# Optimization experiments

Hardware: AMD Instinct MI355X
Metric: run time of the kernel (lower is better)

Reference implementation:

```python
import jax, jax.numpy as jnp
import numpy as np

N = 100000
E = 1600000
F_IN = 3
H = 64


def setup_inputs() -> dict:
    key = jax.random.key(0)
    ks = jax.random.split(key, 12)
    x = jax.random.normal(ks[0], (N, F_IN), dtype=jnp.float32)
    edge_index = jax.random.randint(ks[1], (2, E), 0, N, dtype=jnp.int64)
    def glorot(k, fi, fo):
        s = jnp.sqrt(6.0 / (fi + fo)).astype(jnp.float32)
        return jax.random.uniform(k, (fi, fo), jnp.float32, -s, s)
    return {
        "x": x,
        "edge_index": edge_index,
        "W1": glorot(ks[2], F_IN, H), "b1": jnp.zeros((H,), jnp.float32),
        "W2": glorot(ks[3], H, H),   "b2": jnp.zeros((H,), jnp.float32),
        "W3": glorot(ks[4], H, H),   "b3": jnp.zeros((H,), jnp.float32),
        "Wh": glorot(ks[5], H, 1),   "bh": jnp.zeros((1,), jnp.float32),
    }


def _gcn_conv(x, src, dst, norm, W, b):
    # linear (no bias) -> gather by src -> scale by symmetric norm -> scatter-add to dst -> + bias
    h = x @ W                      # [N, F_out]
    msg = h[src] * norm[:, None]   # [E+N, F_out] (self-loops included)
    out = jax.ops.segment_sum(msg, dst, num_segments=N)
    return out + b


def reference(x, edge_index, W1, b1, W2, b2, W3, b3, Wh, bh):
    # add self-loops (PyG GCNConv default)
    loop = jnp.arange(N, dtype=edge_index.dtype)
    src = jnp.concatenate([edge_index[0], loop])
    dst = jnp.concatenate([edge_index[1], loop])
    # symmetric normalization deg^{-1/2}[src] * deg^{-1/2}[dst]
    deg = jax.ops.segment_sum(jnp.ones_like(dst, dtype=x.dtype), dst, num_segments=N)
    dinv = jnp.where(deg > 0, jax.lax.rsqrt(deg), 0.0)
    norm = dinv[src] * dinv[dst]

    h = _gcn_conv(x, src, dst, norm, W1, b1)
    h = jax.nn.relu(h)  # dropout is identity in eval mode
    h = _gcn_conv(h, src, dst, norm, W2, b2)
    h = jax.nn.relu(h)
    h = _gcn_conv(h, src, dst, norm, W3, b3)
    logits = (h @ Wh + bh).squeeze(-1)  # [N]
    return logits
```

## Files before the change

### kernel.cpp

```cpp
#include <hip/hip_runtime.h>


#define BKSH 8
#define EPB  4096

__device__ __forceinline__ float rlane(float v, int l) {
    return __int_as_float(__builtin_amdgcn_readlane(__float_as_int(v), l));
}
__device__ __forceinline__ int rlane_i(int v, int l) {
    return __builtin_amdgcn_readlane(v, l);
}

__global__ void bhist(const int* __restrict__ dst, int* __restrict__ ghist,
                      int E, int NBK, int BLK) {
    __shared__ int h[512];
    int t = threadIdx.x, b = blockIdx.x;
    for (int i = t; i < NBK; i += 256) h[i] = 0;
    __syncthreads();
    int base = b * EPB;
    #pragma unroll
    for (int i = 0; i < 16; ++i) {
        int e = base + i * 256 + t;
        if (e < E) atomicAdd(&h[dst[e] >> BKSH], 1);
    }
    __syncthreads();
    for (int i = t; i < NBK; i += 256) ghist[(size_t)i * BLK + b] = h[i];
}

__global__ void gscan1(const int* __restrict__ in, int* __restrict__ out,
                       int* __restrict__ bsums, int M) {
    __shared__ int tmp[256];
    int i = blockIdx.x * 256 + threadIdx.x;
    int v = (i < M) ? in[i] : 0;
    tmp[threadIdx.x] = v; __syncthreads();
    for (int off = 1; off < 256; off <<= 1) {
        int t = (threadIdx.x >= off) ? tmp[threadIdx.x - off] : 0;
        __syncthreads();
        tmp[threadIdx.x] += t;
        __syncthreads();
    }
    if (i < M) out[i] = tmp[threadIdx.x] - v;
    if (threadIdx.x == 255) bsums[blockIdx.x] = tmp[255];
}

__global__ void gscan2(int* __restrict__ bsums, int nb) {
    __shared__ int tmp[1024];
    int v = (threadIdx.x < nb) ? bsums[threadIdx.x] : 0;
    tmp[threadIdx.x] = v; __syncthreads();
    for (int off = 1; off < 1024; off <<= 1) {
        int t = (threadIdx.x >= off) ? tmp[threadIdx.x - off] : 0;
        __syncthreads();
        tmp[threadIdx.x] += t;
        __syncthreads();
    }
    if (threadIdx.x < nb) bsums[threadIdx.x] = tmp[threadIdx.x] - v;
}

__global__ void bscatter(const int* __restrict__ src, const int* __restrict__ dst,
                         const int* __restrict__ goff, const int* __restrict__ gbsums,
                         unsigned* __restrict__ tmp, int E, int NBK, int BLK) {
    __shared__ int off[512];
    int t = threadIdx.x, b = blockIdx.x;
    for (int i = t; i < NBK; i += 256) {
        size_t m = (size_t)i * BLK + b;
        off[i] = goff[m] + gbsums[m >> 8];
    }
    __syncthreads();
    int base = b * EPB;
    #pragma unroll
    for (int i = 0; i < 16; ++i) {
        int e = base + i * 256 + t;
        if (e < E) {
            int d = dst[e];
            int p = atomicAdd(&off[d >> BKSH], 1);
            tmp[p] = ((unsigned)src[e] << 8) | (unsigned)(d & 255);
        }
    }
}

__global__ void bucketAF(const unsigned* __restrict__ tmp, const int* __restrict__ goff,
                         const int* __restrict__ gbsums, const float* __restrict__ x,
                         int* __restrict__ rowptr, float* __restrict__ dinv,
                         float4* __restrict__ xd4, int* __restrict__ ewsrc,
                         int N, int NBK, int BLK, int E) {
    __shared__ int lc[256], sc[256], rbase[256];
    int b = blockIdx.x, t = threadIdx.x;
    lc[t] = 0; __syncthreads();
    size_t m0 = (size_t)b * BLK;
    int p0 = goff[m0] + gbsums[m0 >> 8];
    int p1 = E;
    if (b + 1 < NBK) { size_t m1 = (size_t)(b + 1) * BLK; p1 = goff[m1] + gbsums[m1 >> 8]; }
    for (int p = p0 + t; p < p1; p += 256) atomicAdd(&lc[tmp[p] & 255u], 1);
    __syncthreads();
    int v = lc[t];
    sc[t] = v; __syncthreads();
    for (int off = 1; off < 256; off <<= 1) {
        int tv = (t >= off) ? sc[t - off] : 0;
        __syncthreads();
        sc[t] += tv;
        __syncthreads();
    }
    int rb = p0 + (sc[t] - v);
    rbase[t] = rb;
    int node = (b << BKSH) + t;
    if (node < N) {
        rowptr[node] = rb;
        float dvv = rsqrtf((float)(v + 1));
        dinv[node] = dvv;
        xd4[node]  = make_float4(dvv * x[3*node], dvv * x[3*node+1],
                                 dvv * x[3*node+2], 0.f);
    }
    if (b == 0 && t == 0) rowptr[N] = E;
    lc[t] = 0;
    __syncthreads();
    for (int p = p0 + t; p < p1; p += 256) {
        unsigned e = tmp[p];
        int dl = (int)(e & 255u);
        int pos = rbase[dl] + atomicAdd(&lc[dl], 1);
        ewsrc[pos] = (int)(e >> 8);
    }
}

__global__ void agg3w(const int* __restrict__ ewsrc, const int* __restrict__ rowptr,
                      const float* __restrict__ dinv, const float4* __restrict__ xd4,
                      float4* __restrict__ a1, int N) {
    int g   = (blockIdx.x * blockDim.x + threadIdx.x) >> 4;
    int sub = threadIdx.x & 15;
    if (g >= N) return;
    int p0 = rowptr[g], p1 = rowptr[g+1];
    float ax = 0.f, ay = 0.f, az = 0.f;
    for (int p = p0 + sub; p < p1; p += 16) {
        float4 xs = xd4[ewsrc[p]];
        ax += xs.x; ay += xs.y; az += xs.z;
    }
    #pragma unroll
    for (int off = 8; off; off >>= 1) {
        ax += __shfl_down(ax, off, 16);
        ay += __shfl_down(ay, off, 16);
        az += __shfl_down(az, off, 16);
    }
    if (sub == 0) {
        float dv = dinv[g];
        float4 xn = xd4[g];
        a1[g] = make_float4(dv * (ax + xn.x), dv * (ay + xn.y),
                            dv * (az + xn.z), dv);
    }
}

__global__ void fold_head(const float* __restrict__ W3, const float* __restrict__ b3,
                          const float* __restrict__ Wh, const float* __restrict__ bh,
                          float* __restrict__ wc) {
    int k = threadIdx.x;
    float acc = 0.0f;
    for (int f = 0; f < 64; f++) acc += W3[k*64+f] * Wh[f];
    wc[k] = acc;
    if (k == 0) {
        float bb = bh[0];
        for (int f = 0; f < 64; f++) bb += b3[f] * Wh[f];
        wc[64] = bb;
    }
}

__global__ void fused_l2l3(const int* __restrict__ ewsrc, const int* __restrict__ rowptr,
                           const float4* __restrict__ a1, const float* __restrict__ W1,
                           const float* __restrict__ b1, const float* __restrict__ W2,
                           const float* __restrict__ b2, const float* __restrict__ wc,
                           float* __restrict__ zz, int N, int E) {
    __shared__ float Wl[64*64];
    __shared__ float a2buf[4][64];
    const int tid = threadIdx.x;
    for (int i = tid; i < 4096; i += 256) Wl[i] = W2[i];
    const int lane = tid & 63;
    const int wv   = tid >> 6;
    const float w10 = W1[lane], w11 = W1[64+lane], w12 = W1[128+lane];
    const float b1f = b1[lane], b2f = b2[lane], wcf = wc[lane];
    const int NPW = 8;
    const int n0 = (blockIdx.x * 4 + wv) * NPW;
    int   rpl = rowptr[min(n0 + lane, N)];
    float4 sg = a1[min(n0 + lane, N - 1)];
    __syncthreads();
    if (n0 >= N) return;
    for (int cur = 0; cur < NPW; ++cur) {
        int n = n0 + cur;
        if (n >= N) break;
        int p0 = rlane_i(rpl, cur);
        int p1 = rlane_i(rpl, cur + 1);
        float sx = rlane(sg.x, cur), sy = rlane(sg.y, cur);
        float sz2 = rlane(sg.z, cur), sw = rlane(sg.w, cur);
        float ts = fmaf(sz2, w12, fmaf(sy, w11, fmaf(sx, w10, b1f)));
        float acc = sw * fmaxf(ts, 0.f);
        for (int pc = p0; pc < p1; pc += 64) {
            int pidx = pc + lane; if (pidx >= p1) pidx = p1 - 1;
            int s = ewsrc[pidx];
            float4 g = a1[s];
            int m = p1 - pc; if (m > 64) m = 64;
            int j = 0;
            for (; j + 3 < m; j += 4) {
                #pragma unroll
                for (int u = 0; u < 4; ++u) {
                    float ex = rlane(g.x, j+u), ey = rlane(g.y, j+u);
                    float ez = rlane(g.z, j+u), ww = rlane(g.w, j+u);
                    float tt = fmaf(ez, w12, fmaf(ey, w11, fmaf(ex, w10, b1f)));
                    acc = fmaf(ww, fmaxf(tt, 0.f), acc);
                }
            }
            for (; j < m; ++j) {
                float ex = rlane(g.x, j), ey = rlane(g.y, j);
                float ez = rlane(g.z, j), ww = rlane(g.w, j);
                float tt = fmaf(ez, w12, fmaf(ey, w11, fmaf(ex, w10, b1f)));
                acc = fmaf(ww, fmaxf(tt, 0.f), acc);
            }
        }
        acc *= sw;
        a2buf[wv][lane] = acc;
        float h = b2f;
        const float4* a4 = (const float4*)&a2buf[wv][0];
        #pragma unroll
        for (int k4 = 0; k4 < 16; ++k4) {
            float4 a = a4[k4];
            h = fmaf(a.x, Wl[(4*k4+0)*64 + lane], h);
            h = fmaf(a.y, Wl[(4*k4+1)*64 + lane], h);
            h = fmaf(a.z, Wl[(4*k4+2)*64 + lane], h);
            h = fmaf(a.w, Wl[(4*k4+3)*64 + lane], h);
        }
        float v = fmaxf(h, 0.f) * wcf;
        #pragma unroll
        for (int off = 32; off; off >>= 1) v += __shfl_down(v, off);
        if (lane == 0) zz[n] = sw * v;
    }
}

__global__ void final_wave(const float* __restrict__ zz, const int* __restrict__ ewsrc,
                           const int* __restrict__ rowptr, const float* __restrict__ dinv,
                           const float* __restrict__ wc, float* __restrict__ out, int N) {
    int g   = (blockIdx.x * blockDim.x + threadIdx.x) >> 4;
    int sub = threadIdx.x & 15;
    if (g >= N) return;
    int p0 = rowptr[g], p1 = rowptr[g+1];
    float acc = 0.f;
    for (int p = p0 + sub; p < p1; p += 16) {
        acc += zz[ewsrc[p]];
    }
    #pragma unroll
    for (int off = 8; off; off >>= 1) acc += __shfl_down(acc, off, 16);
    if (sub == 0) {
        out[g] = fmaf(dinv[g], zz[g] + acc, wc[64]);
    }
}

extern "C" void kernel_launch(void* const* d_in, const int* in_sizes, int n_in,
                              void* d_out, int out_size, void* d_ws, size_t ws_size,
                              hipStream_t stream) {
    const float* x   = (const float*)d_in[0];
    const int*   ei  = (const int*)d_in[1];
    const float* W1  = (const float*)d_in[2];
    const float* b1  = (const float*)d_in[3];
    const float* W2  = (const float*)d_in[4];
    const float* b2  = (const float*)d_in[5];
    const float* W3  = (const float*)d_in[6];
    const float* b3  = (const float*)d_in[7];
    const float* Wh  = (const float*)d_in[8];
    const float* bh  = (const float*)d_in[9];
    float* logits = (float*)d_out;

    const int N = in_sizes[0] / 3;
    const int E = in_sizes[1] / 2;
    const int* src = ei;
    const int* dst = ei + E;

    const int NBK = (N + 255) >> BKSH;
    const int BLK = (E + EPB - 1) / EPB;
    const int M   = NBK * BLK;

    float* base = (float*)d_ws;
    size_t o = 0;
    float*    dinv   = base + o; o += (size_t)N;
    o = (o + 3) & ~(size_t)3;
    float4*   a1     = (float4*)(base + o); o += (size_t)4*N;
    float4*   xd4    = (float4*)(base + o); o += (size_t)4*N;
    int*      rowptr = (int*)(base + o); o += (size_t)N + 1;
    int*      gbsums = (int*)(base + o); o += 1024;
    int*      ewsrc  = (int*)(base + o); o += (size_t)E;
    unsigned* tmpp   = (unsigned*)(base + o); o += (size_t)E;
    float*    zz     = base + o; o += (size_t)N;
    float*    wc     = base + o; o += 65;
    int*      ghist  = (int*)(base + o); o += (size_t)M;
    int*      goff   = (int*)(base + o); o += (size_t)M;

    const int BS = 256;
    int gM   = (M + BS - 1) / BS;
    int g16  = ((size_t)N * 16 + BS - 1) / BS;
    int gFU  = (N + 31) / 32;

    bhist    <<<BLK, BS, 0, stream>>>(dst, ghist, E, NBK, BLK);
    gscan1   <<<gM,  BS, 0, stream>>>(ghist, goff, gbsums, M);
    gscan2   <<<1, 1024, 0, stream>>>(gbsums, gM);
    bscatter <<<BLK, BS, 0, stream>>>(src, dst, goff, gbsums, tmpp, E, NBK, BLK);
    bucketAF <<<NBK, BS, 0, stream>>>(tmpp, goff, gbsums, x, rowptr, dinv, xd4, ewsrc, N, NBK, BLK, E);
    agg3w    <<<g16, BS, 0, stream>>>(ewsrc, rowptr, dinv, xd4, a1, N);

    fold_head  <<<1, 64, 0, stream>>>(W3, b3, Wh, bh, wc);
    fused_l2l3 <<<gFU, BS, 0, stream>>>(ewsrc, rowptr, a1, W1, b1, W2, b2, wc, zz, N, E);
    final_wave <<<g16, BS, 0, stream>>>(zz, ewsrc, rowptr, dinv, wc, logits, N);
}
```

Baseline: 143.5 us.

## Prefetch next node's neighbor gather and broadcast payload via LDS

In the fused layer-2/3 kernel, the first 64-edge chunk of the next node's neighbors is loaded into registers while the current node is processed, hiding gather latency behind compute. Neighbor payloads are now staged in a per-wave LDS buffer and read back as float4 broadcasts, replacing four readlane operations per edge. Nodes with more than 64 edges fall back to a non-prefetched loop. This adds LDS traffic and relies on wave-synchronous LDS access without an explicit barrier.

```diff
diff --git a/kernel.cpp b/kernel.cpp
--- a/kernel.cpp
+++ b/kernel.cpp
@@ -166,8 +166,9 @@
                            const float* __restrict__ b1, const float* __restrict__ W2,
                            const float* __restrict__ b2, const float* __restrict__ wc,
                            float* __restrict__ zz, int N, int E) {
-    __shared__ float Wl[64*64];
-    __shared__ float a2buf[4][64];
+    __shared__ float  Wl[64*64];
+    __shared__ float4 pay[4][64];
+    __shared__ float  a2buf[4][64];
     const int tid = threadIdx.x;
     for (int i = tid; i < 4096; i += 256) Wl[i] = W2[i];
     const int lane = tid & 63;
@@ -180,35 +181,59 @@
     float4 sg = a1[min(n0 + lane, N - 1)];
     __syncthreads();
     if (n0 >= N) return;
-    for (int cur = 0; cur < NPW; ++cur) {
-        int n = n0 + cur;
-        if (n >= N) break;
-        int p0 = rlane_i(rpl, cur);
-        int p1 = rlane_i(rpl, cur + 1);
+    int NPWv = N - n0; if (NPWv > NPW) NPWv = NPW;
+    int p0c = rlane_i(rpl, 0), p1c = rlane_i(rpl, 1);
+    float4 g_c = make_float4(0.f, 0.f, 0.f, 0.f);
+    if (p0c < p1c) {
+        int pidx = p0c + lane; if (pidx >= p1c) pidx = p1c - 1;
+        g_c = a1[ewsrc[pidx]];
+    }
+    for (int cur = 0; cur < NPWv; ++cur) {
+        int p0 = p0c, p1 = p1c;
+        pay[wv][lane] = g_c;
+        if (cur + 1 < NPWv) {
+            p0c = rlane_i(rpl, cur + 1);
+            p1c = rlane_i(rpl, cur + 2);
+            if (p0c < p1c) {
+                int pidx = p0c + lane; if (pidx >= p1c) pidx = p1c - 1;
+                g_c = a1[ewsrc[pidx]];
+            }
+        }
         float sx = rlane(sg.x, cur), sy = rlane(sg.y, cur);
         float sz2 = rlane(sg.z, cur), sw = rlane(sg.w, cur);
         float ts = fmaf(sz2, w12, fmaf(sy, w11, fmaf(sx, w10, b1f)));
         float acc = sw * fmaxf(ts, 0.f);
-        for (int pc = p0; pc < p1; pc += 64) {
-            int pidx = pc + lane; if (pidx >= p1) pidx = p1 - 1;
-            int s = ewsrc[pidx];
-            float4 g = a1[s];
-            int m = p1 - pc; if (m > 64) m = 64;
+        {
+            int m = p1 - p0; if (m > 64) m = 64;
+            const float4* pp = (const float4*)&pay[wv][0];
             int j = 0;
             for (; j + 3 < m; j += 4) {
-                #pragma unroll
-                for (int u = 0; u < 4; ++u) {
-                    float ex = rlane(g.x, j+u), ey = rlane(g.y, j+u);
-                    float ez = rlane(g.z, j+u), ww = rlane(g.w, j+u);
-                    float tt = fmaf(ez, w12, fmaf(ey, w11, fmaf(ex, w10, b1f)));
-                    acc = fmaf(ww, fmaxf(tt, 0.f), acc);
-                }
+                float4 P0 = pp[j], P1 = pp[j+1], P2 = pp[j+2], P3 = pp[j+3];
+                float t0 = fmaf(P0.z, w12, fmaf(P0.y, w11, fmaf(P0.x, w10, b1f)));
+                float t1 = fmaf(P1.z, w12, fmaf(P1.y, w11, fmaf(P1.x, w10, b1f)));
+                float t2 = fmaf(P2.z, w12, fmaf(P2.y, w11, fmaf(P2.x, w10, b1f)));
+                float t3 = fmaf(P3.z, w12, fmaf(P3.y, w11, fmaf(P3.x, w10, b1f)));
+                acc = fmaf(P0.w, fmaxf(t0, 0.f), acc);
+                acc = fmaf(P1.w, fmaxf(t1, 0.f), acc);
+                acc = fmaf(P2.w, fmaxf(t2, 0.f), acc);
+                acc = fmaf(P3.w, fmaxf(t3, 0.f), acc);
             }
             for (; j < m; ++j) {
-                float ex = rlane(g.x, j), ey = rlane(g.y, j);
-                float ez = rlane(g.z, j), ww = rlane(g.w, j);
-                float tt = fmaf(ez, w12, fmaf(ey, w11, fmaf(ex, w10, b1f)));
-                acc = fmaf(ww, fmaxf(tt, 0.f), acc);
+                float4 P = pp[j];
+                float tt = fmaf(P.z, w12, fmaf(P.y, w11, fmaf(P.x, w10, b1f)));
+                acc = fmaf(P.w, fmaxf(tt, 0.f), acc);
+            }
+        }
+        for (int pc = p0 + 64; pc < p1; pc += 64) {
+            int pidx = pc + lane; if (pidx >= p1) pidx = p1 - 1;
+            float4 g2 = a1[ewsrc[pidx]];
+            pay[wv][lane] = g2;
+            int m2 = p1 - pc; if (m2 > 64) m2 = 64;
+            const float4* pp = (const float4*)&pay[wv][0];
+            for (int j = 0; j < m2; ++j) {
+                float4 P = pp[j];
+                float tt = fmaf(P.z, w12, fmaf(P.y, w11, fmaf(P.x, w10, b1f)));
+                acc = fmaf(P.w, fmaxf(tt, 0.f), acc);
             }
         }
         acc *= sw;
@@ -226,7 +251,7 @@
         float v = fmaxf(h, 0.f) * wcf;
         #pragma unroll
         for (int off = 32; off; off >>= 1) v += __shfl_down(v, off);
-        if (lane == 0) zz[n] = sw * v;
+        if (lane == 0) zz[n0 + cur] = sw * v;
     }
 }
 
```

New measurement: 138.3 us. 3.6% less time.
